# Optimization experiments

Measured on AMD Instinct MI355X. Metric: run time of the kernel, lower is better.

Reference implementation:

```python
import jax, jax.numpy as jnp
import numpy as np

N = 256
D = 1024      # input_dim
C = 256       # class_emb_dim
H = 1024      # hidden_dim
O = 1024      # output_dim
R = 51        # relation_dim
EPS = 1e-5
NEG_SLOPE = 0.01


def setup_inputs() -> dict:
    key = jax.random.key(0)
    ks = jax.random.split(key, 10)
    def kaiming(k, shape):
        fan_in = shape[0]
        return jax.random.normal(k, shape, jnp.float32) * np.sqrt(2.0 / fan_in)
    return {
        "object_feats": jax.random.normal(ks[0], (N, D), jnp.float32),
        "classes_embedding": jax.random.normal(ks[1], (N, N, C), jnp.float32),
        # semantic_encoding: Linear(2D+C, H) -> LeakyReLU -> BatchNorm1d(H) -> Linear(H, O)
        "W1": kaiming(ks[2], (2 * D + C, H)),
        "b1": jnp.zeros((H,), jnp.float32),
        "gamma": jnp.ones((H,), jnp.float32),
        "beta": jnp.zeros((H,), jnp.float32),
        "W2": kaiming(ks[3], (H, O)),
        "b2": jnp.zeros((O,), jnp.float32),
        "w_att": kaiming(ks[4], (O, 1)),
        "b_att": jnp.zeros((1,), jnp.float32),
        "W_rel": kaiming(ks[5], (O, R)),
        "b_rel": jnp.zeros((R,), jnp.float32),
    }


def reference(object_feats, classes_embedding, W1, b1, gamma, beta, W2, b2,
              w_att, b_att, W_rel, b_rel):
    # pair (i, j): concat(feat_i, feat_j, cemb_ij) @ W1  ==
    #   feat_i @ W1[:D] + feat_j @ W1[D:2D] + cemb_ij @ W1[2D:]
    hi = object_feats @ W1[:D]                      # [N, H]
    hj = object_feats @ W1[D:2 * D]                 # [N, H]
    hc = jnp.einsum('nmc,ch->nmh', classes_embedding, W1[2 * D:])  # [N, N, H]
    h = hi[:, None, :] + hj[None, :, :] + hc + b1   # [N, N, H]
    h = jnp.where(h >= 0, h, NEG_SLOPE * h)         # LeakyReLU
    # BatchNorm1d (training mode): batch stats over the N^2 edge batch
    mean = jnp.mean(h, axis=(0, 1))
    var = jnp.mean(jnp.square(h - mean), axis=(0, 1))  # biased var
    h = (h - mean) * jax.lax.rsqrt(var + EPS) * gamma + beta
    feat = h @ W2 + b2                              # [N, N, O] pairwise features
    # attention weights over j, then weighted-sum aggregation
    conf = jnp.squeeze(feat @ w_att, -1) + b_att[0]  # [N, N]
    conf = jax.nn.softmax(conf, axis=1)
    enhanced = jnp.einsum('nm,nmo->no', conf, feat)  # [N, O]
    relation_cls = feat @ W_rel + b_rel              # [N, N, R]
    return feat, enhanced, relation_cls
```

## Files before the change

### kernel.cpp

```cpp
#include <hip/hip_runtime.h>
#include <hip/hip_bf16.h>

typedef __bf16 bf16_t;
typedef __bf16 bf16x8 __attribute__((ext_vector_type(8)));
typedef float  f32x4  __attribute__((ext_vector_type(4)));

#define NNROWS 65536

__device__ __forceinline__ void g2l16(const void* g, void* l) {
  __builtin_amdgcn_global_load_lds(
      (const __attribute__((address_space(1))) void*)g,
      (__attribute__((address_space(3))) void*)l, 16, 0, 0);
}

__global__ __launch_bounds__(256) void k_cvt_cemb(const float* __restrict__ src,
                                                  bf16_t* __restrict__ dst) {
  size_t i = ((size_t)blockIdx.x * 256 + threadIdx.x) * 8;
  float4 t0 = *(const float4*)(src + i);
  float4 t1 = *(const float4*)(src + i + 4);
  bf16x8 v;
  v[0] = (bf16_t)t0.x; v[1] = (bf16_t)t0.y; v[2] = (bf16_t)t0.z; v[3] = (bf16_t)t0.w;
  v[4] = (bf16_t)t1.x; v[5] = (bf16_t)t1.y; v[6] = (bf16_t)t1.z; v[7] = (bf16_t)t1.w;
  *(bf16x8*)(dst + i) = v;
}

__global__ __launch_bounds__(256) void k_w1ct(const float* __restrict__ W1,
                                              bf16_t* __restrict__ W1cT) {
  __shared__ float ls[64][65];
  int t = threadIdx.x;
  int kt = blockIdx.x & 3, nt = blockIdx.x >> 2;
  #pragma unroll
  for (int q = 0; q < 16; ++q) {
    int idx = q * 256 + t, r = idx >> 6, c = idx & 63;
    ls[r][c] = W1[(size_t)(2048 + kt * 64 + r) * 1024 + nt * 64 + c];
  }
  __syncthreads();
  #pragma unroll
  for (int q = 0; q < 16; ++q) {
    int idx = q * 256 + t, nr = idx >> 6, kc = idx & 63;
    W1cT[(size_t)(nt * 64 + nr) * 256 + kt * 64 + kc] = (bf16_t)ls[kc][nr];
  }
}

__global__ __launch_bounds__(256) void k_hihj(const float* __restrict__ feats,
                                              const float* __restrict__ W1,
                                              const float* __restrict__ b1,
                                              float* __restrict__ hi,
                                              float* __restrict__ hj) {
  __shared__ float fs[4][1024];
  int t = threadIdx.x;
  int z = blockIdx.x & 1, ig = blockIdx.x >> 1;
  #pragma unroll
  for (int q = 0; q < 16; ++q) {
    int idx = q * 256 + t, r = idx >> 10, c = idx & 1023;
    fs[r][c] = feats[(size_t)(ig * 4 + r) * 1024 + c];
  }
  __syncthreads();
  float acc[4][4] = {};
  const float* Wz = W1 + (size_t)z * 1024 * 1024;
  for (int k = 0; k < 1024; ++k) {
    float w0 = Wz[(size_t)k * 1024 + t];
    float w1v = Wz[(size_t)k * 1024 + 256 + t];
    float w2v = Wz[(size_t)k * 1024 + 512 + t];
    float w3v = Wz[(size_t)k * 1024 + 768 + t];
    #pragma unroll
    for (int r = 0; r < 4; ++r) {
      float f = fs[r][k];
      acc[r][0] += f * w0; acc[r][1] += f * w1v;
      acc[r][2] += f * w2v; acc[r][3] += f * w3v;
    }
  }
  float* out = z ? hj : hi;
  #pragma unroll
  for (int r = 0; r < 4; ++r)
    #pragma unroll
    for (int q = 0; q < 4; ++q) {
      int n = q * 256 + t;
      float v = acc[r][q];
      if (z == 0) v += b1[n];
      out[(size_t)(ig * 4 + r) * 1024 + n] = v;
    }
}

__global__ __launch_bounds__(256) void k_wrelt(const float* __restrict__ Wrel,
                                               bf16_t* __restrict__ WrelT) {
  int n = blockIdx.x;
  int t = threadIdx.x;
  for (int k = t; k < 1024; k += 256) {
    float v = (n < 51) ? Wrel[(size_t)k * 51 + n] : 0.f;
    WrelT[(size_t)n * 1024 + k] = (bf16_t)v;
  }
}

__global__ __launch_bounds__(256) void k_passA(const bf16_t* __restrict__ Ab,
                                               const bf16_t* __restrict__ Bt,
                                               const float* __restrict__ hi_b1,
                                               const float* __restrict__ hj,
                                               bf16_t* __restrict__ hout,
                                               float* __restrict__ stats) {
  __shared__ bf16_t lsA[128 * 32];
  __shared__ bf16_t lsB[128 * 32];
  const int t = threadIdx.x, lane = t & 63, wid = t >> 6;
  const int wm = wid >> 1, wn = wid & 1;
  int bid = blockIdx.x;
  int swz = (bid & 7) * 512 + (bid >> 3);
  const int bn = swz & 7, bm = swz >> 3;

  const char* gA = (const char*)Ab + (size_t)(bm * 128 + (t >> 2)) * 512 + (t & 3) * 16;
  const char* gB = (const char*)Bt + (size_t)(bn * 128 + (t >> 2)) * 512 + (t & 3) * 16;
  char* lA0 = (char*)lsA + wid * 1024;
  char* lB0 = (char*)lsB + wid * 1024;

  f32x4 acc[4][4];
  #pragma unroll
  for (int a = 0; a < 4; ++a)
    #pragma unroll
    for (int b = 0; b < 4; ++b)
      #pragma unroll
      for (int e = 0; e < 4; ++e) acc[a][b][e] = 0.f;

  for (int kt = 0; kt < 8; ++kt) {
    if (kt) __syncthreads();
    size_t ko = (size_t)kt * 64;
    g2l16(gA + ko, lA0);
    g2l16(gA + ko + (size_t)64 * 512, lA0 + 4096);
    g2l16(gB + ko, lB0);
    g2l16(gB + ko + (size_t)64 * 512, lB0 + 4096);
    __syncthreads();
    const char* pa = (const char*)lsA + (wm * 64 + (lane & 15)) * 64 + (lane >> 4) * 16;
    const char* pb = (const char*)lsB + (wn * 64 + (lane & 15)) * 64 + (lane >> 4) * 16;
    bf16x8 af[4], bfr[4];
    #pragma unroll
    for (int mf = 0; mf < 4; ++mf) af[mf] = *(const bf16x8*)(pa + mf * 1024);
    #pragma unroll
    for (int nf = 0; nf < 4; ++nf) bfr[nf] = *(const bf16x8*)(pb + nf * 1024);
    #pragma unroll
    for (int mf = 0; mf < 4; ++mf)
      #pragma unroll
      for (int nf = 0; nf < 4; ++nf)
        acc[mf][nf] = __builtin_amdgcn_mfma_f32_16x16x32_bf16(af[mf], bfr[nf], acc[mf][nf], 0, 0, 0);
  }

  const int colbase = bn * 128 + wn * 64 + (lane & 15);
  const int i_blk = bm >> 1;
  float hiv[4];
  #pragma unroll
  for (int nf = 0; nf < 4; ++nf) hiv[nf] = hi_b1[(size_t)i_blk * 1024 + colbase + nf * 16];
  float ssum[4] = {0.f, 0.f, 0.f, 0.f}, sq[4] = {0.f, 0.f, 0.f, 0.f};
  #pragma unroll
  for (int mf = 0; mf < 4; ++mf) {
    #pragma unroll
    for (int rg = 0; rg < 4; ++rg) {
      int rl = wm * 64 + mf * 16 + ((lane >> 4) << 2) + rg;
      const float* hjr = hj + (size_t)((bm & 1) * 128 + rl) * 1024;
      bf16_t* ho = hout + (size_t)(bm * 128 + rl) * 1024;
      #pragma unroll
      for (int nf = 0; nf < 4; ++nf) {
        int c = colbase + nf * 16;
        float v = acc[mf][nf][rg] + hiv[nf] + hjr[c];
        v = v >= 0.f ? v : 0.01f * v;
        ho[c] = (bf16_t)v;
        ssum[nf] += v;
        sq[nf] += v * v;
      }
    }
  }
  #pragma unroll
  for (int nf = 0; nf < 4; ++nf) {
    float s = ssum[nf], q = sq[nf];
    s += __shfl_xor(s, 16); q += __shfl_xor(q, 16);
    s += __shfl_xor(s, 32); q += __shfl_xor(q, 32);
    if ((lane >> 4) == 0) {
      atomicAdd(&stats[colbase + nf * 16], s);
      atomicAdd(&stats[1024 + colbase + nf * 16], q);
    }
  }
}

__global__ void k_stats(const float* __restrict__ gamma, const float* __restrict__ beta,
                        const float* __restrict__ b2, const float* __restrict__ stats,
                        float* __restrict__ ab, float* __restrict__ b2p) {
  int k = blockIdx.x * 256 + threadIdx.x;
  float s = stats[k], q = stats[1024 + k];
  float mean = s * (1.f / 65536.f);
  float var = q * (1.f / 65536.f) - mean * mean;
  float a = gamma[k] * rsqrtf(var + 1e-5f);
  float c = beta[k] - mean * a;
  ab[k] = a;
  ab[1024 + k] = c;
  b2p[k] = b2[k];
}

__global__ __launch_bounds__(256) void k_w2pt(const float* __restrict__ W2,
                                              const float* __restrict__ ab,
                                              bf16_t* __restrict__ W2pT,
                                              float* __restrict__ b2p) {
  __shared__ float ls[64][65];
  __shared__ float red[256];
  int t = threadIdx.x;
  int kt = blockIdx.x & 15, nt = blockIdx.x >> 4;
  float cpart = 0.f;
  #pragma unroll
  for (int q = 0; q < 16; ++q) {
    int idx = q * 256 + t, r = idx >> 6, c = idx & 63;
    float v = W2[(size_t)(kt * 64 + r) * 1024 + nt * 64 + c];
    ls[r][c] = v;
    cpart += ab[1024 + kt * 64 + r] * v;
  }
  __syncthreads();
  #pragma unroll
  for (int q = 0; q < 16; ++q) {
    int idx = q * 256 + t, nr = idx >> 6, kc = idx & 63;
    W2pT[(size_t)(nt * 64 + nr) * 1024 + kt * 64 + kc] = (bf16_t)(ab[kt * 64 + kc] * ls[kc][nr]);
  }
  red[t] = cpart;
  __syncthreads();
  if (t < 64) {
    float s2 = red[t] + red[t + 64] + red[t + 128] + red[t + 192];
    atomicAdd(&b2p[nt * 64 + t], s2);
  }
}

__global__ __launch_bounds__(256) void k_passB(const bf16_t* __restrict__ hb,
                                               const bf16_t* __restrict__ W2pT,
                                               const float* __restrict__ b2p,
                                               const float* __restrict__ watt,
                                               float* __restrict__ feat,
                                               float* __restrict__ conf) {
  __shared__ bf16_t lsA[128 * 32];
  __shared__ bf16_t lsB[128 * 32];
  const int t = threadIdx.x, lane = t & 63, wid = t >> 6;
  const int wm = wid >> 1, wn = wid & 1;
  int bid = blockIdx.x;
  int swz = (bid & 7) * 512 + (bid >> 3);
  const int bn = swz & 7, bm = swz >> 3;

  const char* gA = (const char*)hb + (size_t)(bm * 128 + (t >> 2)) * 2048 + (t & 3) * 16;
  const char* gB = (const char*)W2pT + (size_t)(bn * 128 + (t >> 2)) * 2048 + (t & 3) * 16;
  char* lA0 = (char*)lsA + wid * 1024;
  char* lB0 = (char*)lsB + wid * 1024;

  f32x4 acc[4][4];
  #pragma unroll
  for (int a = 0; a < 4; ++a)
    #pragma unroll
    for (int b = 0; b < 4; ++b)
      #pragma unroll
      for (int e = 0; e < 4; ++e) acc[a][b][e] = 0.f;

  for (int kt = 0; kt < 32; ++kt) {
    if (kt) __syncthreads();
    size_t ko = (size_t)kt * 64;
    g2l16(gA + ko, lA0);
    g2l16(gA + ko + (size_t)64 * 2048, lA0 + 4096);
    g2l16(gB + ko, lB0);
    g2l16(gB + ko + (size_t)64 * 2048, lB0 + 4096);
    __syncthreads();
    const char* pa = (const char*)lsA + (wm * 64 + (lane & 15)) * 64 + (lane >> 4) * 16;
    const char* pb = (const char*)lsB + (wn * 64 + (lane & 15)) * 64 + (lane >> 4) * 16;
    bf16x8 af[4], bfr[4];
    #pragma unroll
    for (int mf = 0; mf < 4; ++mf) af[mf] = *(const bf16x8*)(pa + mf * 1024);
    #pragma unroll
    for (int nf = 0; nf < 4; ++nf) bfr[nf] = *(const bf16x8*)(pb + nf * 1024);
    #pragma unroll
    for (int mf = 0; mf < 4; ++mf)
      #pragma unroll
      for (int nf = 0; nf < 4; ++nf)
        acc[mf][nf] = __builtin_amdgcn_mfma_f32_16x16x32_bf16(af[mf], bfr[nf], acc[mf][nf], 0, 0, 0);
  }

  const int colbase = bn * 128 + wn * 64 + (lane & 15);
  const int rowb = bm * 128 + wm * 64 + ((lane >> 4) << 2);
  float b2v[4], wav[4];
  #pragma unroll
  for (int nf = 0; nf < 4; ++nf) {
    int c = colbase + nf * 16;
    b2v[nf] = b2p[c];
    wav[nf] = watt[c];
  }
  #pragma unroll
  for (int mf = 0; mf < 4; ++mf) {
    #pragma unroll
    for (int rg = 0; rg < 4; ++rg) {
      int r = rowb + mf * 16 + rg;
      float* fr = feat + (size_t)r * 1024;
      float cp = 0.f;
      #pragma unroll
      for (int nf = 0; nf < 4; ++nf) {
        float v = acc[mf][nf][rg] + b2v[nf];
        fr[colbase + nf * 16] = v;
        cp += v * wav[nf];
      }
      cp += __shfl_xor(cp, 1); cp += __shfl_xor(cp, 2);
      cp += __shfl_xor(cp, 4); cp += __shfl_xor(cp, 8);
      if ((lane & 15) == 0) atomicAdd(&conf[r], cp);
    }
  }
}

__global__ __launch_bounds__(256) void k_softmax(float* __restrict__ conf) {
  __shared__ float red[8];
  int i = blockIdx.x, t = threadIdx.x;
  float x = conf[i * 256 + t];
  float m = x;
  #pragma unroll
  for (int d = 1; d < 64; d <<= 1) m = fmaxf(m, __shfl_xor(m, d));
  if ((t & 63) == 0) red[t >> 6] = m;
  __syncthreads();
  m = fmaxf(fmaxf(red[0], red[1]), fmaxf(red[2], red[3]));
  float e = __expf(x - m);
  float s = e;
  #pragma unroll
  for (int d = 1; d < 64; d <<= 1) s += __shfl_xor(s, d);
  if ((t & 63) == 0) red[4 + (t >> 6)] = s;
  __syncthreads();
  s = red[4] + red[5] + red[6] + red[7];
  conf[i * 256 + t] = e / s;
}

__global__ __launch_bounds__(256) void k_enh(const float* __restrict__ feat,
                                             const float* __restrict__ conf,
                                             float* __restrict__ out) {
  __shared__ float cw[256];
  int bid = blockIdx.x, i = bid >> 2, oc = bid & 3;
  int t = threadIdx.x;
  cw[t] = conf[i * 256 + t];
  __syncthreads();
  const float* fp = feat + (size_t)i * 256 * 1024 + oc * 256 + t;
  float a = 0.f;
  #pragma unroll 4
  for (int j = 0; j < 256; ++j) a += cw[j] * fp[(size_t)j * 1024];
  out[(size_t)i * 1024 + oc * 256 + t] = a;
}

__global__ __launch_bounds__(256) void k_rel(const float* __restrict__ feat,
                                             const bf16_t* __restrict__ WrelT,
                                             const float* __restrict__ brel,
                                             float* __restrict__ out) {
  const int t = threadIdx.x, lane = t & 63, w = t >> 6;
  const int r0 = blockIdx.x * 64 + w * 16;
  const float* ap = feat + (size_t)(r0 + (lane & 15)) * 1024 + ((lane >> 4) << 3);
  const bf16_t* bp = WrelT + (size_t)(lane & 15) * 1024 + ((lane >> 4) << 3);
  f32x4 acc[4];
  #pragma unroll
  for (int nf = 0; nf < 4; ++nf)
    #pragma unroll
    for (int e = 0; e < 4; ++e) acc[nf][e] = 0.f;
  for (int kt = 0; kt < 32; ++kt) {
    float4 t0 = *(const float4*)(ap + kt * 32);
    float4 t1 = *(const float4*)(ap + kt * 32 + 4);
    bf16x8 af;
    af[0] = (bf16_t)t0.x; af[1] = (bf16_t)t0.y; af[2] = (bf16_t)t0.z; af[3] = (bf16_t)t0.w;
    af[4] = (bf16_t)t1.x; af[5] = (bf16_t)t1.y; af[6] = (bf16_t)t1.z; af[7] = (bf16_t)t1.w;
    #pragma unroll
    for (int nf = 0; nf < 4; ++nf) {
      bf16x8 bfr = *(const bf16x8*)(bp + (size_t)nf * 16 * 1024 + kt * 32);
      acc[nf] = __builtin_amdgcn_mfma_f32_16x16x32_bf16(af, bfr, acc[nf], 0, 0, 0);
    }
  }
  #pragma unroll
  for (int nf = 0; nf < 4; ++nf) {
    int c = nf * 16 + (lane & 15);
    if (c < 51) {
      float bb = brel[c];
      #pragma unroll
      for (int rg = 0; rg < 4; ++rg) {
        int rr = r0 + ((lane >> 4) << 2) + rg;
        out[(size_t)rr * 51 + c] = acc[nf][rg] + bb;
      }
    }
  }
}

extern "C" void kernel_launch(void* const* d_in, const int* in_sizes, int n_in,
                              void* d_out, int out_size, void* d_ws, size_t ws_size,
                              hipStream_t stream) {
  const float* feats = (const float*)d_in[0];
  const float* cemb  = (const float*)d_in[1];
  const float* W1    = (const float*)d_in[2];
  const float* b1    = (const float*)d_in[3];
  const float* gamma = (const float*)d_in[4];
  const float* beta  = (const float*)d_in[5];
  const float* W2    = (const float*)d_in[6];
  const float* b2    = (const float*)d_in[7];
  const float* watt  = (const float*)d_in[8];
  const float* Wrel  = (const float*)d_in[10];
  const float* brel  = (const float*)d_in[11];

  float* feat = (float*)d_out;
  float* enh  = (float*)d_out + (size_t)67108864;
  float* rel  = (float*)d_out + (size_t)67371008;

  char* ws = (char*)d_ws;
  bf16_t* h     = (bf16_t*)(ws + 0);
  bf16_t* cembb = (bf16_t*)(ws + 134217728);
  bf16_t* W1cT  = (bf16_t*)(ws + 167772160);
  bf16_t* W2pT  = (bf16_t*)(ws + 168296448);
  bf16_t* WrelT = (bf16_t*)(ws + 170393600);
  float*  hi    = (float*)(ws + 170524672);
  float*  hj    = (float*)(ws + 171573248);
  float*  stats = (float*)(ws + 172621824);
  float*  ab    = (float*)(ws + 172630016);
  float*  b2p   = (float*)(ws + 172638208);
  float*  conf  = (float*)(ws + 172642304);

  hipMemsetAsync(stats, 0, 2 * 1024 * sizeof(float), stream);
  hipMemsetAsync(conf, 0, (size_t)65536 * sizeof(float), stream);

  k_cvt_cemb<<<8192, 256, 0, stream>>>(cemb, cembb);
  k_w1ct<<<64, 256, 0, stream>>>(W1, W1cT);
  k_hihj<<<128, 256, 0, stream>>>(feats, W1, b1, hi, hj);
  k_wrelt<<<64, 256, 0, stream>>>(Wrel, WrelT);
  k_passA<<<4096, 256, 0, stream>>>(cembb, W1cT, hi, hj, h, stats);
  k_stats<<<4, 256, 0, stream>>>(gamma, beta, b2, stats, ab, b2p);
  k_w2pt<<<256, 256, 0, stream>>>(W2, ab, W2pT, b2p);
  k_passB<<<4096, 256, 0, stream>>>(h, W2pT, b2p, watt, feat, conf);
  k_softmax<<<256, 256, 0, stream>>>(conf);
  k_enh<<<1024, 256, 0, stream>>>(feat, conf, enh);
  k_rel<<<1024, 256, 0, stream>>>(feat, WrelT, brel, rel);
}
```

Before: 912.6 us.

## Fuse cemb conversion into passA and refactor enh/rel via algebraic reassociation

```diff
diff --git a/kernel.cpp b/kernel.cpp
--- a/kernel.cpp
+++ b/kernel.cpp
@@ -4,24 +4,11 @@
 typedef __bf16 bf16_t;
 typedef __bf16 bf16x8 __attribute__((ext_vector_type(8)));
 typedef float  f32x4  __attribute__((ext_vector_type(4)));
-
-#define NNROWS 65536
 
 __device__ __forceinline__ void g2l16(const void* g, void* l) {
   __builtin_amdgcn_global_load_lds(
       (const __attribute__((address_space(1))) void*)g,
       (__attribute__((address_space(3))) void*)l, 16, 0, 0);
-}
-
-__global__ __launch_bounds__(256) void k_cvt_cemb(const float* __restrict__ src,
-                                                  bf16_t* __restrict__ dst) {
-  size_t i = ((size_t)blockIdx.x * 256 + threadIdx.x) * 8;
-  float4 t0 = *(const float4*)(src + i);
-  float4 t1 = *(const float4*)(src + i + 4);
-  bf16x8 v;
-  v[0] = (bf16_t)t0.x; v[1] = (bf16_t)t0.y; v[2] = (bf16_t)t0.z; v[3] = (bf16_t)t0.w;
-  v[4] = (bf16_t)t1.x; v[5] = (bf16_t)t1.y; v[6] = (bf16_t)t1.z; v[7] = (bf16_t)t1.w;
-  *(bf16x8*)(dst + i) = v;
 }
 
 __global__ __launch_bounds__(256) void k_w1ct(const float* __restrict__ W1,
@@ -82,17 +69,22 @@
     }
 }
 
-__global__ __launch_bounds__(256) void k_wrelt(const float* __restrict__ Wrel,
-                                               bf16_t* __restrict__ WrelT) {
-  int n = blockIdx.x;
+__global__ __launch_bounds__(256) void k_wc(const float* __restrict__ W2,
+                                            const float* __restrict__ Wrel,
+                                            float* __restrict__ M) {
   int t = threadIdx.x;
-  for (int k = t; k < 1024; k += 256) {
-    float v = (n < 51) ? Wrel[(size_t)k * 51 + n] : 0.f;
-    WrelT[(size_t)n * 1024 + k] = (bf16_t)v;
-  }
-}
-
-__global__ __launch_bounds__(256) void k_passA(const bf16_t* __restrict__ Ab,
+  int r = t & 63, kl = t >> 6;
+  int k = blockIdx.x * 4 + kl;
+  float acc = 0.f;
+  if (r < 51) {
+    const float* w2r = W2 + (size_t)k * 1024;
+    #pragma unroll 4
+    for (int o = 0; o < 1024; ++o) acc += w2r[o] * Wrel[(size_t)o * 51 + r];
+  }
+  M[(size_t)k * 64 + r] = acc;
+}
+
+__global__ __launch_bounds__(256) void k_passA(const float* __restrict__ cemb,
                                                const bf16_t* __restrict__ Bt,
                                                const float* __restrict__ hi_b1,
                                                const float* __restrict__ hj,
@@ -106,9 +98,9 @@
   int swz = (bid & 7) * 512 + (bid >> 3);
   const int bn = swz & 7, bm = swz >> 3;
 
-  const char* gA = (const char*)Ab + (size_t)(bm * 128 + (t >> 2)) * 512 + (t & 3) * 16;
+  const float* gAf = cemb + (size_t)(bm * 128 + (t >> 1)) * 256 + (t & 1) * 16;
   const char* gB = (const char*)Bt + (size_t)(bn * 128 + (t >> 2)) * 512 + (t & 3) * 16;
-  char* lA0 = (char*)lsA + wid * 1024;
+  char* lAw = (char*)lsA + (t >> 1) * 64 + (t & 1) * 32;
   char* lB0 = (char*)lsB + wid * 1024;
 
   f32x4 acc[4][4];
@@ -121,11 +113,17 @@
 
   for (int kt = 0; kt < 8; ++kt) {
     if (kt) __syncthreads();
-    size_t ko = (size_t)kt * 64;
-    g2l16(gA + ko, lA0);
-    g2l16(gA + ko + (size_t)64 * 512, lA0 + 4096);
-    g2l16(gB + ko, lB0);
-    g2l16(gB + ko + (size_t)64 * 512, lB0 + 4096);
+    const float4* fp = (const float4*)(gAf + kt * 32);
+    float4 f0 = fp[0], f1 = fp[1], f2 = fp[2], f3 = fp[3];
+    g2l16(gB + (size_t)kt * 64, lB0);
+    g2l16(gB + (size_t)kt * 64 + (size_t)64 * 512, lB0 + 4096);
+    bf16x8 w0, w1;
+    w0[0] = (bf16_t)f0.x; w0[1] = (bf16_t)f0.y; w0[2] = (bf16_t)f0.z; w0[3] = (bf16_t)f0.w;
+    w0[4] = (bf16_t)f1.x; w0[5] = (bf16_t)f1.y; w0[6] = (bf16_t)f1.z; w0[7] = (bf16_t)f1.w;
+    w1[0] = (bf16_t)f2.x; w1[1] = (bf16_t)f2.y; w1[2] = (bf16_t)f2.z; w1[3] = (bf16_t)f2.w;
+    w1[4] = (bf16_t)f3.x; w1[5] = (bf16_t)f3.y; w1[6] = (bf16_t)f3.z; w1[7] = (bf16_t)f3.w;
+    *(bf16x8*)lAw = w0;
+    *(bf16x8*)(lAw + 16) = w1;
     __syncthreads();
     const char* pa = (const char*)lsA + (wm * 64 + (lane & 15)) * 64 + (lane >> 4) * 16;
     const char* pb = (const char*)lsB + (wn * 64 + (lane & 15)) * 64 + (lane >> 4) * 16;
@@ -218,6 +216,28 @@
   if (t < 64) {
     float s2 = red[t] + red[t + 64] + red[t + 128] + red[t + 192];
     atomicAdd(&b2p[nt * 64 + t], s2);
+  }
+}
+
+__global__ __launch_bounds__(256) void k_wct(const float* __restrict__ ab,
+                                             const float* __restrict__ M,
+                                             const float* __restrict__ b2p,
+                                             const float* __restrict__ Wrel,
+                                             const float* __restrict__ brel,
+                                             bf16_t* __restrict__ WcT,
+                                             float* __restrict__ brelp) {
+  __shared__ float rd[4];
+  int n = blockIdx.x, t = threadIdx.x;
+  for (int k = t; k < 1024; k += 256)
+    WcT[(size_t)n * 1024 + k] = (bf16_t)(ab[k] * M[(size_t)k * 64 + n]);
+  if (n < 51) {
+    float p = 0.f;
+    for (int o = t; o < 1024; o += 256) p += b2p[o] * Wrel[(size_t)o * 51 + n];
+    p += __shfl_xor(p, 1); p += __shfl_xor(p, 2); p += __shfl_xor(p, 4);
+    p += __shfl_xor(p, 8); p += __shfl_xor(p, 16); p += __shfl_xor(p, 32);
+    if ((t & 63) == 0) rd[t >> 6] = p;
+    __syncthreads();
+    if (t == 0) brelp[n] = rd[0] + rd[1] + rd[2] + rd[3] + brel[n];
   }
 }
 
@@ -319,29 +339,44 @@
   conf[i * 256 + t] = e / s;
 }
 
-__global__ __launch_bounds__(256) void k_enh(const float* __restrict__ feat,
+__global__ __launch_bounds__(256) void k_cwh(const bf16_t* __restrict__ h,
                                              const float* __restrict__ conf,
-                                             float* __restrict__ out) {
-  __shared__ float cw[256];
-  int bid = blockIdx.x, i = bid >> 2, oc = bid & 3;
-  int t = threadIdx.x;
-  cw[t] = conf[i * 256 + t];
-  __syncthreads();
-  const float* fp = feat + (size_t)i * 256 * 1024 + oc * 256 + t;
-  float a = 0.f;
-  #pragma unroll 4
-  for (int j = 0; j < 256; ++j) a += cw[j] * fp[(size_t)j * 1024];
-  out[(size_t)i * 1024 + oc * 256 + t] = a;
-}
-
-__global__ __launch_bounds__(256) void k_rel(const float* __restrict__ feat,
-                                             const bf16_t* __restrict__ WrelT,
-                                             const float* __restrict__ brel,
-                                             float* __restrict__ out) {
+                                             float* __restrict__ cwh) {
+  __shared__ float cf[256];
+  __shared__ float part[128 * 8];
+  int i = blockIdx.x, t = threadIdx.x;
+  cf[t] = conf[i * 256 + t];
+  __syncthreads();
+  int o0 = (t & 127) * 8, jh = t >> 7;
+  const bf16_t* hp = h + (size_t)i * 262144 + (size_t)jh * 131072 + o0;
+  float a[8] = {};
+  for (int j = 0; j < 128; ++j) {
+    bf16x8 v = *(const bf16x8*)(hp + (size_t)j * 1024);
+    float c = cf[jh * 128 + j];
+    #pragma unroll
+    for (int e = 0; e < 8; ++e) a[e] += c * (float)v[e];
+  }
+  if (jh == 1) {
+    #pragma unroll
+    for (int e = 0; e < 8; ++e) part[(t & 127) * 8 + e] = a[e];
+  }
+  __syncthreads();
+  if (jh == 0) {
+    #pragma unroll
+    for (int e = 0; e < 8; ++e)
+      cwh[(size_t)i * 1024 + o0 + e] = a[e] + part[(t & 127) * 8 + e];
+  }
+}
+
+__global__ __launch_bounds__(256) void k_enh2(const float* __restrict__ cwh,
+                                              const bf16_t* __restrict__ W2pT,
+                                              const float* __restrict__ b2p,
+                                              float* __restrict__ out) {
   const int t = threadIdx.x, lane = t & 63, w = t >> 6;
-  const int r0 = blockIdx.x * 64 + w * 16;
-  const float* ap = feat + (size_t)(r0 + (lane & 15)) * 1024 + ((lane >> 4) << 3);
-  const bf16_t* bp = WrelT + (size_t)(lane & 15) * 1024 + ((lane >> 4) << 3);
+  const int rb = blockIdx.x >> 4, cb = blockIdx.x & 15;
+  const int r0 = rb * 64 + w * 16;
+  const float* ap = cwh + (size_t)(r0 + (lane & 15)) * 1024 + ((lane >> 4) << 3);
+  const bf16_t* bp = W2pT + (size_t)(cb * 64 + (lane & 15)) * 1024 + ((lane >> 4) << 3);
   f32x4 acc[4];
   #pragma unroll
   for (int nf = 0; nf < 4; ++nf)
@@ -361,9 +396,42 @@
   }
   #pragma unroll
   for (int nf = 0; nf < 4; ++nf) {
+    int c = cb * 64 + nf * 16 + (lane & 15);
+    float bb = b2p[c];
+    #pragma unroll
+    for (int rg = 0; rg < 4; ++rg) {
+      int rr = r0 + ((lane >> 4) << 2) + rg;
+      out[(size_t)rr * 1024 + c] = acc[nf][rg] + bb;
+    }
+  }
+}
+
+__global__ __launch_bounds__(256) void k_rel(const bf16_t* __restrict__ h,
+                                             const bf16_t* __restrict__ WcT,
+                                             const float* __restrict__ brelp,
+                                             float* __restrict__ out) {
+  const int t = threadIdx.x, lane = t & 63, w = t >> 6;
+  const int r0 = blockIdx.x * 64 + w * 16;
+  const bf16_t* ap = h + (size_t)(r0 + (lane & 15)) * 1024 + ((lane >> 4) << 3);
+  const bf16_t* bp = WcT + (size_t)(lane & 15) * 1024 + ((lane >> 4) << 3);
+  f32x4 acc[4];
+  #pragma unroll
+  for (int nf = 0; nf < 4; ++nf)
+    #pragma unroll
+    for (int e = 0; e < 4; ++e) acc[nf][e] = 0.f;
+  for (int kt = 0; kt < 32; ++kt) {
+    bf16x8 af = *(const bf16x8*)(ap + kt * 32);
+    #pragma unroll
+    for (int nf = 0; nf < 4; ++nf) {
+      bf16x8 bfr = *(const bf16x8*)(bp + (size_t)nf * 16 * 1024 + kt * 32);
+      acc[nf] = __builtin_amdgcn_mfma_f32_16x16x32_bf16(af, bfr, acc[nf], 0, 0, 0);
+    }
+  }
+  #pragma unroll
+  for (int nf = 0; nf < 4; ++nf) {
     int c = nf * 16 + (lane & 15);
     if (c < 51) {
-      float bb = brel[c];
+      float bb = brelp[c];
       #pragma unroll
       for (int rg = 0; rg < 4; ++rg) {
         int rr = r0 + ((lane >> 4) << 2) + rg;
@@ -394,29 +462,32 @@
 
   char* ws = (char*)d_ws;
   bf16_t* h     = (bf16_t*)(ws + 0);
-  bf16_t* cembb = (bf16_t*)(ws + 134217728);
-  bf16_t* W1cT  = (bf16_t*)(ws + 167772160);
-  bf16_t* W2pT  = (bf16_t*)(ws + 168296448);
-  bf16_t* WrelT = (bf16_t*)(ws + 170393600);
-  float*  hi    = (float*)(ws + 170524672);
-  float*  hj    = (float*)(ws + 171573248);
-  float*  stats = (float*)(ws + 172621824);
-  float*  ab    = (float*)(ws + 172630016);
-  float*  b2p   = (float*)(ws + 172638208);
-  float*  conf  = (float*)(ws + 172642304);
+  bf16_t* W1cT  = (bf16_t*)(ws + 134217728);
+  bf16_t* W2pT  = (bf16_t*)(ws + 134742016);
+  bf16_t* WcT   = (bf16_t*)(ws + 136839168);
+  float*  M     = (float*)(ws + 136970240);
+  float*  hi    = (float*)(ws + 137232384);
+  float*  hj    = (float*)(ws + 138280960);
+  float*  stats = (float*)(ws + 139329536);
+  float*  ab    = (float*)(ws + 139337728);
+  float*  b2p   = (float*)(ws + 139345920);
+  float*  brelp = (float*)(ws + 139350016);
+  float*  conf  = (float*)(ws + 139350528);
+  float*  cwh   = (float*)(ws + 139612672);
 
   hipMemsetAsync(stats, 0, 2 * 1024 * sizeof(float), stream);
   hipMemsetAsync(conf, 0, (size_t)65536 * sizeof(float), stream);
 
-  k_cvt_cemb<<<8192, 256, 0, stream>>>(cemb, cembb);
   k_w1ct<<<64, 256, 0, stream>>>(W1, W1cT);
   k_hihj<<<128, 256, 0, stream>>>(feats, W1, b1, hi, hj);
-  k_wrelt<<<64, 256, 0, stream>>>(Wrel, WrelT);
-  k_passA<<<4096, 256, 0, stream>>>(cembb, W1cT, hi, hj, h, stats);
+  k_wc<<<256, 256, 0, stream>>>(W2, Wrel, M);
+  k_passA<<<4096, 256, 0, stream>>>(cemb, W1cT, hi, hj, h, stats);
   k_stats<<<4, 256, 0, stream>>>(gamma, beta, b2, stats, ab, b2p);
   k_w2pt<<<256, 256, 0, stream>>>(W2, ab, W2pT, b2p);
+  k_wct<<<64, 256, 0, stream>>>(ab, M, b2p, Wrel, brel, WcT, brelp);
   k_passB<<<4096, 256, 0, stream>>>(h, W2pT, b2p, watt, feat, conf);
   k_softmax<<<256, 256, 0, stream>>>(conf);
-  k_enh<<<1024, 256, 0, stream>>>(feat, conf, enh);
-  k_rel<<<1024, 256, 0, stream>>>(feat, WrelT, brel, rel);
-}
+  k_cwh<<<256, 256, 0, stream>>>(h, conf, cwh);
+  k_enh2<<<64, 256, 0, stream>>>(cwh, W2pT, b2p, enh);
+  k_rel<<<1024, 256, 0, stream>>>(h, WcT, brelp, rel);
+}
```

Result: slower. 1.030 ms (+12.8%).
